# Kernel optimization log

Hardware: AMD Instinct MI355X
Metric: run time of the kernel (lower is better)

The kernel has to match this reference:

```python
import jax, jax.numpy as jnp
import numpy as np

B, S = 16384, 2048
EPS = 1e-8


def _autocorr(x, lag):
    # Pearson correlation between x[:, :-lag] and x[:, lag:] (ddof cancels).
    a = x[:, :-lag]
    b = x[:, lag:]
    am = a.mean(axis=1, keepdims=True)
    bm = b.mean(axis=1, keepdims=True)
    cov = ((a - am) * (b - bm)).mean(axis=1)
    return cov / (a.std(axis=1) * b.std(axis=1))


def _stat_features(x):
    S_len = x.shape[1]
    mean = x.mean(axis=1)
    xc = x - mean[:, None]
    m2 = (xc ** 2).mean(axis=1)
    m3 = (xc ** 3).mean(axis=1)
    m4 = (xc ** 4).mean(axis=1)
    std = jnp.sqrt(m2)
    min_v = x.min(axis=1)
    max_v = x.max(axis=1)
    q = jnp.percentile(x, jnp.array([25.0, 50.0, 75.0]), axis=1)  # [3, B]
    p25, median, p75 = q[0], q[1], q[2]
    diff = jnp.diff(x, axis=1)
    std_diff = diff.std(axis=1)
    trend = std_diff / (std + EPS)
    ac1 = _autocorr(x, 1)
    ac7 = _autocorr(x, 7)
    ac24 = _autocorr(x, 24)
    cv = std / (jnp.abs(mean) + EPS)
    iqr = p75 - p25
    seasonal = x[:, ::24].var(axis=1) / (m2 + EPS)
    skew = m3 / (m2 ** 1.5)          # scipy.stats.skew, bias=True
    kurt = m4 / (m2 ** 2) - 3.0      # scipy.stats.kurtosis, Fisher, bias=True
    length = jnp.full_like(mean, float(S_len))
    sum_abs_diff = jnp.abs(diff).sum(axis=1)
    mean_abs_diff = jnp.abs(diff).mean(axis=1)
    feats = jnp.stack([mean, std, min_v, max_v, median, trend, ac1, ac7, ac24,
                       cv, iqr, seasonal, skew, kurt, length,
                       sum_abs_diff, mean_abs_diff, std_diff, p25, p75], axis=1)
    return jnp.where(jnp.isfinite(feats), feats, 0.0)


def setup_inputs() -> dict:
    key = jax.random.key(0)
    k0, k1, k2, k3, k4 = jax.random.split(key, 5)
    x = jax.random.normal(k0, (B, S), dtype=jnp.float32)
    W1 = jax.random.normal(k1, (64, 20), dtype=jnp.float32) * 0.1
    b1 = jnp.zeros((64,), dtype=jnp.float32)
    W2 = jax.random.normal(k3, (128, 64), dtype=jnp.float32) * 0.1
    b2 = jnp.zeros((128,), dtype=jnp.float32)
    return {"x": x, "W1": W1, "b1": b1, "W2": W2, "b2": b2}


def reference(x, W1, b1, W2, b2):
    feats = _stat_features(x)                      # [B, 20]
    h = jax.nn.relu(feats @ W1.T + b1)             # [B, 64] (dropout inactive at eval)
    return h @ W2.T + b2                           # [B, 128]
```

## Files before the change

### kernel.cpp

```cpp
#include <hip/hip_runtime.h>
#include <cmath>

constexpr int S_LEN = 2048;
constexpr float EPS = 1e-8f;

typedef unsigned uvec32 __attribute__((ext_vector_type(32)));

__device__ __forceinline__ float fin(float v) { return isfinite(v) ? v : 0.0f; }
__device__ __forceinline__ float rcpf(float x) { return __builtin_amdgcn_rcpf(x); }

__device__ __forceinline__ unsigned f2o_bits(unsigned u) {
    return (u & 0x80000000u) ? ~u : (u | 0x80000000u);
}
__device__ __forceinline__ float o2f(unsigned u) {
    return __uint_as_float((u & 0x80000000u) ? (u ^ 0x80000000u) : ~u);
}

template <int Ctrl, int Rmask>
__device__ __forceinline__ int dpp_zero_i(int x) {
    return __builtin_amdgcn_update_dpp(0, x, Ctrl, Rmask, 0xF, true);
}
template <int Ctrl>
__device__ __forceinline__ int dpp_keep_i(int x) {
    return __builtin_amdgcn_update_dpp(x, x, Ctrl, 0xF, 0xF, false);
}
__device__ __forceinline__ float dpp_shdn1_f(float x) {
    return __uint_as_float((unsigned)dpp_zero_i<0x130, 0xF>((int)__float_as_uint(x)));
}
__device__ __forceinline__ int wred_add_i(int v) {
    v += dpp_zero_i<0xB1, 0xF>(v);
    v += dpp_zero_i<0x4E, 0xF>(v);
    v += dpp_zero_i<0x114, 0xF>(v);
    v += dpp_zero_i<0x118, 0xF>(v);
    v += dpp_zero_i<0x142, 0xA>(v);
    v += dpp_zero_i<0x143, 0xC>(v);
    return __builtin_amdgcn_readlane(v, 63);
}
__device__ __forceinline__ float wred_add_f(float v) {
    #define ADDF(CT, RM) v += __uint_as_float((unsigned)dpp_zero_i<CT, RM>((int)__float_as_uint(v)))
    ADDF(0xB1, 0xF); ADDF(0x4E, 0xF); ADDF(0x114, 0xF);
    ADDF(0x118, 0xF); ADDF(0x142, 0xA); ADDF(0x143, 0xC);
    #undef ADDF
    return __uint_as_float((unsigned)__builtin_amdgcn_readlane((int)__float_as_uint(v), 63));
}
__device__ __forceinline__ float wred_min_f(float v) {
    #define MINF(CT) v = fminf(v, __uint_as_float((unsigned)dpp_keep_i<CT>((int)__float_as_uint(v))))
    MINF(0xB1); MINF(0x4E); MINF(0x114); MINF(0x118); MINF(0x142); MINF(0x143);
    #undef MINF
    return __uint_as_float((unsigned)__builtin_amdgcn_readlane((int)__float_as_uint(v), 63));
}
__device__ __forceinline__ float wred_max_f(float v) {
    #define MAXF(CT) v = fmaxf(v, __uint_as_float((unsigned)dpp_keep_i<CT>((int)__float_as_uint(v))))
    MAXF(0xB1); MAXF(0x4E); MAXF(0x114); MAXF(0x118); MAXF(0x142); MAXF(0x143);
    #undef MAXF
    return __uint_as_float((unsigned)__builtin_amdgcn_readlane((int)__float_as_uint(v), 63));
}
__device__ __forceinline__ unsigned wred_umin(unsigned v) {
    #define MINU(CT) { unsigned t = (unsigned)dpp_keep_i<CT>((int)v); v = v < t ? v : t; }
    MINU(0xB1) MINU(0x4E) MINU(0x114) MINU(0x118) MINU(0x142) MINU(0x143)
    #undef MINU
    return (unsigned)__builtin_amdgcn_readlane((int)v, 63);
}
__device__ __forceinline__ float readlane_f(float x, int l) {
    return __uint_as_float((unsigned)__builtin_amdgcn_readlane((int)__float_as_uint(x), l));
}

__device__ __forceinline__ void transpose32(uvec32& A) {
    #pragma unroll
    for (int k = 0; k < 16; k++) {
        unsigned lo = __builtin_amdgcn_perm(A[k], A[k + 16], 0x07060302u);
        unsigned hi = __builtin_amdgcn_perm(A[k], A[k + 16], 0x05040100u);
        A[k] = lo; A[k + 16] = hi;
    }
    #pragma unroll
    for (int k0 = 0; k0 < 32; k0 += 16) {
        #pragma unroll
        for (int k = k0; k < k0 + 8; k++) {
            unsigned lo = __builtin_amdgcn_perm(A[k], A[k + 8], 0x07030501u);
            unsigned hi = __builtin_amdgcn_perm(A[k], A[k + 8], 0x06020400u);
            A[k] = lo; A[k + 8] = hi;
        }
    }
    #pragma unroll
    for (int j = 4; j; j >>= 1) {
        const unsigned m = (j == 4) ? 0x0F0F0F0Fu : (j == 2) ? 0x33333333u : 0x55555555u;
        #pragma unroll
        for (int k = 0; k < 32; k++) {
            if (!(k & j)) {
                unsigned Ak = A[k], Bk = A[k | j];
                A[k]     = ((Bk >> j) & m) | (Ak & ~m);
                A[k | j] = ((Ak << j) & ~m) | (Bk & m);
            }
        }
    }
}

#define VF(e) __uint_as_float(a[e])

__global__ __launch_bounds__(256) void transpose_w_kernel(
    const float* __restrict__ W1, float* __restrict__ wt)
{
    int tid = blockIdx.x * blockDim.x + threadIdx.x;
    int stride = gridDim.x * blockDim.x;
    for (int n = tid; n < 64 * 20; n += stride) {
        int j = n & 63, k = n >> 6;
        wt[n] = W1[j * 20 + k];
    }
}

__global__ __launch_bounds__(256, 5) void fused_stats_mlp_kernel(
    const float* __restrict__ x, const float* __restrict__ wt,
    const float* __restrict__ b1, const float* __restrict__ W2,
    const float* __restrict__ b2, float* __restrict__ out, int nrows)
{
    __shared__ __align__(16) float sf[4][20];
    __shared__ __align__(16) float hsh[4][64];

    const int gw   = (blockIdx.x * 256 + threadIdx.x) >> 6;
    const int lane = threadIdx.x & 63;
    const int w    = (threadIdx.x >> 6);
    if (gw >= nrows) return;

    uvec32 a;
    const float* xr = x + (size_t)gw * S_LEN + lane * 32;
    #pragma unroll
    for (int q = 0; q < 8; q++) {
        float4 t = reinterpret_cast<const float4*>(xr)[q];
        a[4 * q + 0] = __float_as_uint(t.x); a[4 * q + 1] = __float_as_uint(t.y);
        a[4 * q + 2] = __float_as_uint(t.z); a[4 * q + 3] = __float_as_uint(t.w);
    }

    float s1 = 0.f, s2 = 0.f, s3 = 0.f, s4 = 0.f, sd2 = 0.f, sad = 0.f;
    float p1 = 0.f, p7 = 0.f, p24 = 0.f, se1 = 0.f, se2 = 0.f;
    float mn = VF(0), mx = VF(0);
    #pragma unroll
    for (int e = 0; e < 32; e++) {
        float val = VF(e);
        float t = val * val;
        s1 += val; s2 += t;
        s3 = fmaf(t, val, s3); s4 = fmaf(t, t, s4);
        mn = fminf(mn, val); mx = fmaxf(mx, val);
    }
    #pragma unroll
    for (int e = 0; e < 31; e++) {
        float d = VF(e + 1) - VF(e);
        sd2 = fmaf(d, d, sd2); sad += fabsf(d);
        p1 = fmaf(VF(e), VF(e + 1), p1);
    }
    #pragma unroll
    for (int e = 0; e < 25; e++) p7 = fmaf(VF(e), VF(e + 7), p7);
    #pragma unroll
    for (int e = 0; e < 8; e++)  p24 = fmaf(VF(e), VF(e + 24), p24);

    const bool notlast = (lane < 63);
    #pragma unroll
    for (int j = 0; j < 24; j++) {
        float g = dpp_shdn1_f(VF(j));
        p24 = fmaf(VF(8 + j), g, p24);
        if (j < 7) p7 = fmaf(VF(25 + j), g, p7);
        if (j == 0) {
            float d = g - VF(31);
            float dm = notlast ? d : 0.f;
            sd2 = fmaf(dm, dm, sd2); sad += fabsf(dm);
            p1 = fmaf(VF(31), g, p1);
        }
    }
    {
        int r3 = lane % 3;
        float sv = (r3 == 0) ? VF(0) : ((r3 == 1) ? VF(16) : VF(8));
        se1 += sv; se2 = fmaf(sv, sv, se2);
        if (r3 == 0) { se1 += VF(24); se2 = fmaf(VF(24), VF(24), se2); }
    }
    const bool is63 = (lane == 63);
    float acc1 = 0.f, acc2 = 0.f, ck1 = 0.f, ck2 = 0.f;
    #pragma unroll
    for (int i = 0; i < 24; i++) {
        float pick = is63 ? VF(31 - i) : VF(i);
        acc1 += pick; acc2 = fmaf(pick, pick, acc2);
        if (i == 6) { ck1 = acc1; ck2 = acc2; }
    }
    const float h1  = readlane_f(VF(0), 0),   t1  = readlane_f(VF(31), 63);
    const float h7  = readlane_f(ck1, 0),     hq7 = readlane_f(ck2, 0);
    const float h24 = readlane_f(acc1, 0),    hq24 = readlane_f(acc2, 0);
    const float t7  = readlane_f(ck1, 63),    tq7 = readlane_f(ck2, 63);
    const float t24 = readlane_f(acc1, 63),   tq24 = readlane_f(acc2, 63);
    const float hq1 = h1 * h1, tq1 = t1 * t1;

    float S1  = wred_add_f(s1);
    float S2  = wred_add_f(s2);
    float S3  = wred_add_f(s3);
    float S4  = wred_add_f(s4);
    float SD2 = wred_add_f(sd2);
    float SAD = wred_add_f(sad);
    float P1  = wred_add_f(p1);
    float P7  = wred_add_f(p7);
    float P24 = wred_add_f(p24);
    float SE1 = wred_add_f(se1);
    float SE2 = wred_add_f(se2);
    float MN  = wred_min_f(mn);
    float MX  = wred_max_f(mx);

    {
        constexpr float invS  = 1.0f / 2048.0f;
        constexpr float invND = 1.0f / 2047.0f;
        const float Sf = (float)S_LEN;
        float mu = S1 * invS;
        float q2 = S2 * invS, q3 = S3 * invS, q4 = S4 * invS;
        float mu2 = mu * mu;
        float m2v = q2 - mu2;
        float m3v = q3 - 3.f * mu * q2 + 2.f * mu * mu2;
        float m4v = q4 - 4.f * mu * q3 + 6.f * mu2 * q2 - 3.f * mu2 * mu2;
        float stdv = sqrtf(m2v);
        float dmean = (t1 - h1) * invND;
        float dvar = SD2 * invND - dmean * dmean;
        float std_diff = sqrtf(fmaxf(dvar, 0.f));
        float trend = std_diff * rcpf(stdv + EPS);
        float ac[3];
        const float invN[3] = {1.0f / 2047.0f, 1.0f / 2041.0f, 1.0f / 2024.0f};
        const float Ps[3] = {P1, P7, P24};
        const float hd[3] = {h1, h7, h24},   hqv[3] = {hq1, hq7, hq24};
        const float tl[3] = {t1, t7, t24},   tqv[3] = {tq1, tq7, tq24};
        #pragma unroll
        for (int q = 0; q < 3; q++) {
            float in = invN[q];
            float sa = S1 - tl[q], sb = S1 - hd[q];
            float qa = S2 - tqv[q], qb = S2 - hqv[q];
            float am = sa * in, bm = sb * in;
            float cov = Ps[q] * in - am * bm;
            float as_ = sqrtf(fmaxf(qa * in - am * am, 0.f));
            float bs_ = sqrtf(fmaxf(qb * in - bm * bm, 0.f));
            ac[q] = cov * rcpf(as_ * bs_);
        }
        float cv = stdv * rcpf(fabsf(mu) + EPS);
        float sm = SE1 * (1.0f / 86.0f);
        float svar = SE2 * (1.0f / 86.0f) - sm * sm;
        float seasonal = svar * rcpf(m2v + EPS);
        float skew = m3v * rcpf(m2v * stdv);
        float kurt = m4v * rcpf(m2v * m2v) - 3.f;
        if (lane == 0) {
            float* s = sf[w];
            s[0]  = fin(mu);       s[1]  = fin(stdv);
            s[2]  = fin(MN);       s[3]  = fin(MX);
            s[5]  = fin(trend);    s[6]  = fin(ac[0]);
            s[7]  = fin(ac[1]);    s[8]  = fin(ac[2]);
            s[9]  = fin(cv);       s[11] = fin(seasonal);
            s[12] = fin(skew);     s[13] = fin(kurt);
            s[14] = Sf;            s[15] = fin(SAD);
            s[16] = fin(SAD * invND); s[17] = fin(std_diff);
        }
    }

    #pragma unroll
    for (int e = 0; e < 32; e++) a[e] = f2o_bits(a[e]);
    transpose32(a);

    unsigned act0 = ~0u, act1 = ~0u, act2 = ~0u;
    int K0 = 511, K1 = 1023, K2 = 1535;
    int cnt0 = 2048, cnt1 = 2048, cnt2 = 2048;
    unsigned uK0 = 0, uK1 = 0, uK2 = 0;
    #pragma unroll
    for (int b = 31; b >= 0; b--) {
        unsigned mb = a[31 - b];
        unsigned w0 = act0 & mb, w1 = act1 & mb, w2 = act2 & mb;
        int O01 = wred_add_i(__popc(w0) | (__popc(w1) << 16));
        int O2  = wred_add_i(__popc(w2));
        int c0 = cnt0 - (O01 & 0xFFFF);
        int c1 = cnt1 - (int)((unsigned)O01 >> 16);
        int c2i = cnt2 - O2;
        bool t0 = (K0 >= c0), t1c = (K1 >= c1), t2c = (K2 >= c2i);
        act0 = t0  ? w0 : (act0 ^ w0);
        act1 = t1c ? w1 : (act1 ^ w1);
        act2 = t2c ? w2 : (act2 ^ w2);
        cnt0 = t0  ? (cnt0 - c0)  : c0;
        cnt1 = t1c ? (cnt1 - c1)  : c1;
        cnt2 = t2c ? (cnt2 - c2i) : c2i;
        K0 = t0  ? (K0 - c0)  : K0;
        K1 = t1c ? (K1 - c1)  : K1;
        K2 = t2c ? (K2 - c2i) : K2;
        uK0 |= t0  ? (1u << b) : 0u;
        uK1 |= t1c ? (1u << b) : 0u;
        uK2 |= t2c ? (1u << b) : 0u;
    }
    const int eq0 = cnt0, eq1 = cnt1, eq2 = cnt2;

    transpose32(a);
    const unsigned k0p1 = uK0 + 1, k1p1 = uK1 + 1, k2p1 = uK2 + 1;
    unsigned m0 = ~0u, m1 = ~0u, m2 = ~0u;
    #pragma unroll
    for (int e = 0; e < 32; e++) {
        unsigned ue = a[e];
        unsigned d0 = ue - k0p1; m0 = m0 < d0 ? m0 : d0;
        unsigned d1 = ue - k1p1; m1 = m1 < d1 ? m1 : d1;
        unsigned d2 = ue - k2p1; m2 = m2 < d2 ? m2 : d2;
    }
    m0 = wred_umin(m0) + k0p1;
    m1 = wred_umin(m1) + k1p1;
    m2 = wred_umin(m2) + k2p1;

    float v511 = o2f(uK0), v1023 = o2f(uK1), v1535 = o2f(uK2);
    float v512  = (K0 + 1 < eq0) ? v511  : o2f(m0);
    float v1024 = (K1 + 1 < eq1) ? v1023 : o2f(m1);
    float v1536 = (K2 + 1 < eq2) ? v1535 : o2f(m2);
    float p25 = v511 + 0.75f * (v512 - v511);
    float med = 0.5f * (v1023 + v1024);
    float p75 = v1535 + 0.25f * (v1536 - v1535);
    float iqr = p75 - p25;

    if (lane == 0) {
        float* s = sf[w];
        s[4]  = fin(med); s[10] = fin(iqr);
        s[18] = fin(p25); s[19] = fin(p75);
    }
    __asm__ volatile("s_waitcnt lgkmcnt(0)" ::: "memory");
    __builtin_amdgcn_sched_barrier(0);

    const float* W1T = wt;
    const float4* sfv = (const float4*)sf[w];
    float4 f0 = sfv[0], f1 = sfv[1], f2 = sfv[2], f3 = sfv[3], f4 = sfv[4];
    float h = b1[lane];
    h = fmaf(f0.x, W1T[ 0 * 64 + lane], h);
    h = fmaf(f0.y, W1T[ 1 * 64 + lane], h);
    h = fmaf(f0.z, W1T[ 2 * 64 + lane], h);
    h = fmaf(f0.w, W1T[ 3 * 64 + lane], h);
    h = fmaf(f1.x, W1T[ 4 * 64 + lane], h);
    h = fmaf(f1.y, W1T[ 5 * 64 + lane], h);
    h = fmaf(f1.z, W1T[ 6 * 64 + lane], h);
    h = fmaf(f1.w, W1T[ 7 * 64 + lane], h);
    h = fmaf(f2.x, W1T[ 8 * 64 + lane], h);
    h = fmaf(f2.y, W1T[ 9 * 64 + lane], h);
    h = fmaf(f2.z, W1T[10 * 64 + lane], h);
    h = fmaf(f2.w, W1T[11 * 64 + lane], h);
    h = fmaf(f3.x, W1T[12 * 64 + lane], h);
    h = fmaf(f3.y, W1T[13 * 64 + lane], h);
    h = fmaf(f3.z, W1T[14 * 64 + lane], h);
    h = fmaf(f3.w, W1T[15 * 64 + lane], h);
    h = fmaf(f4.x, W1T[16 * 64 + lane], h);
    h = fmaf(f4.y, W1T[17 * 64 + lane], h);
    h = fmaf(f4.z, W1T[18 * 64 + lane], h);
    h = fmaf(f4.w, W1T[19 * 64 + lane], h);
    h = fmaxf(h, 0.f);
    hsh[w][lane] = h;
    __asm__ volatile("s_waitcnt lgkmcnt(0)" ::: "memory");
    __builtin_amdgcn_sched_barrier(0);

    const int j2 = lane * 2;
    float2 b2v = *(const float2*)(b2 + j2);
    float acc0 = b2v.x, acc1b = b2v.y;
    const float4* w2r0 = (const float4*)(W2 + (size_t)j2 * 64);
    const float4* w2r1 = (const float4*)(W2 + (size_t)(j2 + 1) * 64);
    const float4* hv4 = (const float4*)hsh[w];
    #pragma unroll
    for (int q = 0; q < 16; q++) {
        float4 hq = hv4[q];
        float4 wa = w2r0[q];
        float4 wb = w2r1[q];
        acc0 = fmaf(hq.x, wa.x, acc0); acc1b = fmaf(hq.x, wb.x, acc1b);
        acc0 = fmaf(hq.y, wa.y, acc0); acc1b = fmaf(hq.y, wb.y, acc1b);
        acc0 = fmaf(hq.z, wa.z, acc0); acc1b = fmaf(hq.z, wb.z, acc1b);
        acc0 = fmaf(hq.w, wa.w, acc0); acc1b = fmaf(hq.w, wb.w, acc1b);
    }
    *(float2*)(out + (size_t)gw * 128 + j2) = make_float2(acc0, acc1b);
}

extern "C" void kernel_launch(void* const* d_in, const int* in_sizes, int n_in,
                              void* d_out, int out_size, void* d_ws, size_t ws_size,
                              hipStream_t stream) {
    const float* x  = (const float*)d_in[0];
    const float* W1 = (const float*)d_in[1];
    const float* b1 = (const float*)d_in[2];
    const float* W2 = (const float*)d_in[3];
    const float* b2 = (const float*)d_in[4];
    float* out = (float*)d_out;
    float* wt  = (float*)d_ws;
    int nrows = in_sizes[0] / S_LEN;
    int blocks = (nrows + 3) / 4;
    transpose_w_kernel<<<2, 256, 0, stream>>>(W1, wt);
    fused_stats_mlp_kernel<<<blocks, 256, 0, stream>>>(x, wt, b1, W2, b2, out, nrows);
}
```

Before: 266.4 us.

## Process two rows per wavefront with interleaved radix select and early exit

Each wavefront now loads and processes two rows, and the bitwise radix-select passes for both rows are interleaved so their cross-lane reductions can overlap and hide latency. The bit loop exits early once every quantile candidate set has shrunk to one element, and an extra min-distance pass snaps the partial prefix to the actual element value. Launch bounds drop to 4 waves per SIMD because holding two 32-element rows in registers raises register pressure, and half as many blocks are launched.

```diff
diff --git a/kernel.cpp b/kernel.cpp
--- a/kernel.cpp
+++ b/kernel.cpp
@@ -95,47 +95,15 @@
     }
 }
 
-#define VF(e) __uint_as_float(a[e])
-
-__global__ __launch_bounds__(256) void transpose_w_kernel(
-    const float* __restrict__ W1, float* __restrict__ wt)
-{
-    int tid = blockIdx.x * blockDim.x + threadIdx.x;
-    int stride = gridDim.x * blockDim.x;
-    for (int n = tid; n < 64 * 20; n += stride) {
-        int j = n & 63, k = n >> 6;
-        wt[n] = W1[j * 20 + k];
-    }
-}
-
-__global__ __launch_bounds__(256, 5) void fused_stats_mlp_kernel(
-    const float* __restrict__ x, const float* __restrict__ wt,
-    const float* __restrict__ b1, const float* __restrict__ W2,
-    const float* __restrict__ b2, float* __restrict__ out, int nrows)
-{
-    __shared__ __align__(16) float sf[4][20];
-    __shared__ __align__(16) float hsh[4][64];
-
-    const int gw   = (blockIdx.x * 256 + threadIdx.x) >> 6;
-    const int lane = threadIdx.x & 63;
-    const int w    = (threadIdx.x >> 6);
-    if (gw >= nrows) return;
-
-    uvec32 a;
-    const float* xr = x + (size_t)gw * S_LEN + lane * 32;
-    #pragma unroll
-    for (int q = 0; q < 8; q++) {
-        float4 t = reinterpret_cast<const float4*>(xr)[q];
-        a[4 * q + 0] = __float_as_uint(t.x); a[4 * q + 1] = __float_as_uint(t.y);
-        a[4 * q + 2] = __float_as_uint(t.z); a[4 * q + 3] = __float_as_uint(t.w);
-    }
-
+#define AF(e) __uint_as_float(a[e])
+
+__device__ __forceinline__ void phase1_stats(const uvec32& a, float* s, int lane) {
     float s1 = 0.f, s2 = 0.f, s3 = 0.f, s4 = 0.f, sd2 = 0.f, sad = 0.f;
     float p1 = 0.f, p7 = 0.f, p24 = 0.f, se1 = 0.f, se2 = 0.f;
-    float mn = VF(0), mx = VF(0);
+    float mn = AF(0), mx = AF(0);
     #pragma unroll
     for (int e = 0; e < 32; e++) {
-        float val = VF(e);
+        float val = AF(e);
         float t = val * val;
         s1 += val; s2 += t;
         s3 = fmaf(t, val, s3); s4 = fmaf(t, t, s4);
@@ -143,43 +111,43 @@
     }
     #pragma unroll
     for (int e = 0; e < 31; e++) {
-        float d = VF(e + 1) - VF(e);
+        float d = AF(e + 1) - AF(e);
         sd2 = fmaf(d, d, sd2); sad += fabsf(d);
-        p1 = fmaf(VF(e), VF(e + 1), p1);
-    }
-    #pragma unroll
-    for (int e = 0; e < 25; e++) p7 = fmaf(VF(e), VF(e + 7), p7);
-    #pragma unroll
-    for (int e = 0; e < 8; e++)  p24 = fmaf(VF(e), VF(e + 24), p24);
+        p1 = fmaf(AF(e), AF(e + 1), p1);
+    }
+    #pragma unroll
+    for (int e = 0; e < 25; e++) p7 = fmaf(AF(e), AF(e + 7), p7);
+    #pragma unroll
+    for (int e = 0; e < 8; e++)  p24 = fmaf(AF(e), AF(e + 24), p24);
 
     const bool notlast = (lane < 63);
     #pragma unroll
     for (int j = 0; j < 24; j++) {
-        float g = dpp_shdn1_f(VF(j));
-        p24 = fmaf(VF(8 + j), g, p24);
-        if (j < 7) p7 = fmaf(VF(25 + j), g, p7);
+        float g = dpp_shdn1_f(AF(j));
+        p24 = fmaf(AF(8 + j), g, p24);
+        if (j < 7) p7 = fmaf(AF(25 + j), g, p7);
         if (j == 0) {
-            float d = g - VF(31);
+            float d = g - AF(31);
             float dm = notlast ? d : 0.f;
             sd2 = fmaf(dm, dm, sd2); sad += fabsf(dm);
-            p1 = fmaf(VF(31), g, p1);
+            p1 = fmaf(AF(31), g, p1);
         }
     }
     {
         int r3 = lane % 3;
-        float sv = (r3 == 0) ? VF(0) : ((r3 == 1) ? VF(16) : VF(8));
+        float sv = (r3 == 0) ? AF(0) : ((r3 == 1) ? AF(16) : AF(8));
         se1 += sv; se2 = fmaf(sv, sv, se2);
-        if (r3 == 0) { se1 += VF(24); se2 = fmaf(VF(24), VF(24), se2); }
+        if (r3 == 0) { se1 += AF(24); se2 = fmaf(AF(24), AF(24), se2); }
     }
     const bool is63 = (lane == 63);
     float acc1 = 0.f, acc2 = 0.f, ck1 = 0.f, ck2 = 0.f;
     #pragma unroll
     for (int i = 0; i < 24; i++) {
-        float pick = is63 ? VF(31 - i) : VF(i);
+        float pick = is63 ? AF(31 - i) : AF(i);
         acc1 += pick; acc2 = fmaf(pick, pick, acc2);
         if (i == 6) { ck1 = acc1; ck2 = acc2; }
     }
-    const float h1  = readlane_f(VF(0), 0),   t1  = readlane_f(VF(31), 63);
+    const float h1  = readlane_f(AF(0), 0),   t1  = readlane_f(AF(31), 63);
     const float h7  = readlane_f(ck1, 0),     hq7 = readlane_f(ck2, 0);
     const float h24 = readlane_f(acc1, 0),    hq24 = readlane_f(acc2, 0);
     const float t7  = readlane_f(ck1, 63),    tq7 = readlane_f(ck2, 63);
@@ -200,146 +168,84 @@
     float MN  = wred_min_f(mn);
     float MX  = wred_max_f(mx);
 
-    {
-        constexpr float invS  = 1.0f / 2048.0f;
-        constexpr float invND = 1.0f / 2047.0f;
-        const float Sf = (float)S_LEN;
-        float mu = S1 * invS;
-        float q2 = S2 * invS, q3 = S3 * invS, q4 = S4 * invS;
-        float mu2 = mu * mu;
-        float m2v = q2 - mu2;
-        float m3v = q3 - 3.f * mu * q2 + 2.f * mu * mu2;
-        float m4v = q4 - 4.f * mu * q3 + 6.f * mu2 * q2 - 3.f * mu2 * mu2;
-        float stdv = sqrtf(m2v);
-        float dmean = (t1 - h1) * invND;
-        float dvar = SD2 * invND - dmean * dmean;
-        float std_diff = sqrtf(fmaxf(dvar, 0.f));
-        float trend = std_diff * rcpf(stdv + EPS);
-        float ac[3];
-        const float invN[3] = {1.0f / 2047.0f, 1.0f / 2041.0f, 1.0f / 2024.0f};
-        const float Ps[3] = {P1, P7, P24};
-        const float hd[3] = {h1, h7, h24},   hqv[3] = {hq1, hq7, hq24};
-        const float tl[3] = {t1, t7, t24},   tqv[3] = {tq1, tq7, tq24};
-        #pragma unroll
-        for (int q = 0; q < 3; q++) {
-            float in = invN[q];
-            float sa = S1 - tl[q], sb = S1 - hd[q];
-            float qa = S2 - tqv[q], qb = S2 - hqv[q];
-            float am = sa * in, bm = sb * in;
-            float cov = Ps[q] * in - am * bm;
-            float as_ = sqrtf(fmaxf(qa * in - am * am, 0.f));
-            float bs_ = sqrtf(fmaxf(qb * in - bm * bm, 0.f));
-            ac[q] = cov * rcpf(as_ * bs_);
-        }
-        float cv = stdv * rcpf(fabsf(mu) + EPS);
-        float sm = SE1 * (1.0f / 86.0f);
-        float svar = SE2 * (1.0f / 86.0f) - sm * sm;
-        float seasonal = svar * rcpf(m2v + EPS);
-        float skew = m3v * rcpf(m2v * stdv);
-        float kurt = m4v * rcpf(m2v * m2v) - 3.f;
-        if (lane == 0) {
-            float* s = sf[w];
-            s[0]  = fin(mu);       s[1]  = fin(stdv);
-            s[2]  = fin(MN);       s[3]  = fin(MX);
-            s[5]  = fin(trend);    s[6]  = fin(ac[0]);
-            s[7]  = fin(ac[1]);    s[8]  = fin(ac[2]);
-            s[9]  = fin(cv);       s[11] = fin(seasonal);
-            s[12] = fin(skew);     s[13] = fin(kurt);
-            s[14] = Sf;            s[15] = fin(SAD);
-            s[16] = fin(SAD * invND); s[17] = fin(std_diff);
-        }
-    }
-
-    #pragma unroll
-    for (int e = 0; e < 32; e++) a[e] = f2o_bits(a[e]);
-    transpose32(a);
-
-    unsigned act0 = ~0u, act1 = ~0u, act2 = ~0u;
-    int K0 = 511, K1 = 1023, K2 = 1535;
-    int cnt0 = 2048, cnt1 = 2048, cnt2 = 2048;
-    unsigned uK0 = 0, uK1 = 0, uK2 = 0;
-    #pragma unroll
-    for (int b = 31; b >= 0; b--) {
-        unsigned mb = a[31 - b];
-        unsigned w0 = act0 & mb, w1 = act1 & mb, w2 = act2 & mb;
-        int O01 = wred_add_i(__popc(w0) | (__popc(w1) << 16));
-        int O2  = wred_add_i(__popc(w2));
-        int c0 = cnt0 - (O01 & 0xFFFF);
-        int c1 = cnt1 - (int)((unsigned)O01 >> 16);
-        int c2i = cnt2 - O2;
-        bool t0 = (K0 >= c0), t1c = (K1 >= c1), t2c = (K2 >= c2i);
-        act0 = t0  ? w0 : (act0 ^ w0);
-        act1 = t1c ? w1 : (act1 ^ w1);
-        act2 = t2c ? w2 : (act2 ^ w2);
-        cnt0 = t0  ? (cnt0 - c0)  : c0;
-        cnt1 = t1c ? (cnt1 - c1)  : c1;
-        cnt2 = t2c ? (cnt2 - c2i) : c2i;
-        K0 = t0  ? (K0 - c0)  : K0;
-        K1 = t1c ? (K1 - c1)  : K1;
-        K2 = t2c ? (K2 - c2i) : K2;
-        uK0 |= t0  ? (1u << b) : 0u;
-        uK1 |= t1c ? (1u << b) : 0u;
-        uK2 |= t2c ? (1u << b) : 0u;
-    }
-    const int eq0 = cnt0, eq1 = cnt1, eq2 = cnt2;
-
-    transpose32(a);
-    const unsigned k0p1 = uK0 + 1, k1p1 = uK1 + 1, k2p1 = uK2 + 1;
-    unsigned m0 = ~0u, m1 = ~0u, m2 = ~0u;
-    #pragma unroll
-    for (int e = 0; e < 32; e++) {
-        unsigned ue = a[e];
-        unsigned d0 = ue - k0p1; m0 = m0 < d0 ? m0 : d0;
-        unsigned d1 = ue - k1p1; m1 = m1 < d1 ? m1 : d1;
-        unsigned d2 = ue - k2p1; m2 = m2 < d2 ? m2 : d2;
-    }
-    m0 = wred_umin(m0) + k0p1;
-    m1 = wred_umin(m1) + k1p1;
-    m2 = wred_umin(m2) + k2p1;
-
-    float v511 = o2f(uK0), v1023 = o2f(uK1), v1535 = o2f(uK2);
-    float v512  = (K0 + 1 < eq0) ? v511  : o2f(m0);
-    float v1024 = (K1 + 1 < eq1) ? v1023 : o2f(m1);
-    float v1536 = (K2 + 1 < eq2) ? v1535 : o2f(m2);
-    float p25 = v511 + 0.75f * (v512 - v511);
-    float med = 0.5f * (v1023 + v1024);
-    float p75 = v1535 + 0.25f * (v1536 - v1535);
-    float iqr = p75 - p25;
-
+    constexpr float invS  = 1.0f / 2048.0f;
+    constexpr float invND = 1.0f / 2047.0f;
+    const float Sf = (float)S_LEN;
+    float mu = S1 * invS;
+    float q2 = S2 * invS, q3 = S3 * invS, q4 = S4 * invS;
+    float mu2 = mu * mu;
+    float m2v = q2 - mu2;
+    float m3v = q3 - 3.f * mu * q2 + 2.f * mu * mu2;
+    float m4v = q4 - 4.f * mu * q3 + 6.f * mu2 * q2 - 3.f * mu2 * mu2;
+    float stdv = sqrtf(m2v);
+    float dmean = (t1 - h1) * invND;
+    float dvar = SD2 * invND - dmean * dmean;
+    float std_diff = sqrtf(fmaxf(dvar, 0.f));
+    float trend = std_diff * rcpf(stdv + EPS);
+    float ac[3];
+    const float invN[3] = {1.0f / 2047.0f, 1.0f / 2041.0f, 1.0f / 2024.0f};
+    const float Ps[3] = {P1, P7, P24};
+    const float hd[3] = {h1, h7, h24},   hqv[3] = {hq1, hq7, hq24};
+    const float tl[3] = {t1, t7, t24},   tqv[3] = {tq1, tq7, tq24};
+    #pragma unroll
+    for (int q = 0; q < 3; q++) {
+        float in = invN[q];
+        float sa = S1 - tl[q], sb = S1 - hd[q];
+        float qa = S2 - tqv[q], qb = S2 - hqv[q];
+        float am = sa * in, bm = sb * in;
+        float cov = Ps[q] * in - am * bm;
+        float as_ = sqrtf(fmaxf(qa * in - am * am, 0.f));
+        float bs_ = sqrtf(fmaxf(qb * in - bm * bm, 0.f));
+        ac[q] = cov * rcpf(as_ * bs_);
+    }
+    float cv = stdv * rcpf(fabsf(mu) + EPS);
+    float sm = SE1 * (1.0f / 86.0f);
+    float svar = SE2 * (1.0f / 86.0f) - sm * sm;
+    float seasonal = svar * rcpf(m2v + EPS);
+    float skew = m3v * rcpf(m2v * stdv);
+    float kurt = m4v * rcpf(m2v * m2v) - 3.f;
     if (lane == 0) {
-        float* s = sf[w];
-        s[4]  = fin(med); s[10] = fin(iqr);
-        s[18] = fin(p25); s[19] = fin(p75);
-    }
-    __asm__ volatile("s_waitcnt lgkmcnt(0)" ::: "memory");
-    __builtin_amdgcn_sched_barrier(0);
-
-    const float* W1T = wt;
-    const float4* sfv = (const float4*)sf[w];
+        s[0]  = fin(mu);       s[1]  = fin(stdv);
+        s[2]  = fin(MN);       s[3]  = fin(MX);
+        s[5]  = fin(trend);    s[6]  = fin(ac[0]);
+        s[7]  = fin(ac[1]);    s[8]  = fin(ac[2]);
+        s[9]  = fin(cv);       s[11] = fin(seasonal);
+        s[12] = fin(skew);     s[13] = fin(kurt);
+        s[14] = Sf;            s[15] = fin(SAD);
+        s[16] = fin(SAD * invND); s[17] = fin(std_diff);
+    }
+}
+
+__device__ __forceinline__ void mlp_row(
+    const float* __restrict__ wt, const float* __restrict__ b1,
+    const float* __restrict__ W2, const float* __restrict__ b2,
+    const float* sfrow, float* hrow, float* __restrict__ outrow, int lane)
+{
+    const float4* sfv = (const float4*)sfrow;
     float4 f0 = sfv[0], f1 = sfv[1], f2 = sfv[2], f3 = sfv[3], f4 = sfv[4];
     float h = b1[lane];
-    h = fmaf(f0.x, W1T[ 0 * 64 + lane], h);
-    h = fmaf(f0.y, W1T[ 1 * 64 + lane], h);
-    h = fmaf(f0.z, W1T[ 2 * 64 + lane], h);
-    h = fmaf(f0.w, W1T[ 3 * 64 + lane], h);
-    h = fmaf(f1.x, W1T[ 4 * 64 + lane], h);
-    h = fmaf(f1.y, W1T[ 5 * 64 + lane], h);
-    h = fmaf(f1.z, W1T[ 6 * 64 + lane], h);
-    h = fmaf(f1.w, W1T[ 7 * 64 + lane], h);
-    h = fmaf(f2.x, W1T[ 8 * 64 + lane], h);
-    h = fmaf(f2.y, W1T[ 9 * 64 + lane], h);
-    h = fmaf(f2.z, W1T[10 * 64 + lane], h);
-    h = fmaf(f2.w, W1T[11 * 64 + lane], h);
-    h = fmaf(f3.x, W1T[12 * 64 + lane], h);
-    h = fmaf(f3.y, W1T[13 * 64 + lane], h);
-    h = fmaf(f3.z, W1T[14 * 64 + lane], h);
-    h = fmaf(f3.w, W1T[15 * 64 + lane], h);
-    h = fmaf(f4.x, W1T[16 * 64 + lane], h);
-    h = fmaf(f4.y, W1T[17 * 64 + lane], h);
-    h = fmaf(f4.z, W1T[18 * 64 + lane], h);
-    h = fmaf(f4.w, W1T[19 * 64 + lane], h);
+    h = fmaf(f0.x, wt[ 0 * 64 + lane], h);
+    h = fmaf(f0.y, wt[ 1 * 64 + lane], h);
+    h = fmaf(f0.z, wt[ 2 * 64 + lane], h);
+    h = fmaf(f0.w, wt[ 3 * 64 + lane], h);
+    h = fmaf(f1.x, wt[ 4 * 64 + lane], h);
+    h = fmaf(f1.y, wt[ 5 * 64 + lane], h);
+    h = fmaf(f1.z, wt[ 6 * 64 + lane], h);
+    h = fmaf(f1.w, wt[ 7 * 64 + lane], h);
+    h = fmaf(f2.x, wt[ 8 * 64 + lane], h);
+    h = fmaf(f2.y, wt[ 9 * 64 + lane], h);
+    h = fmaf(f2.z, wt[10 * 64 + lane], h);
+    h = fmaf(f2.w, wt[11 * 64 + lane], h);
+    h = fmaf(f3.x, wt[12 * 64 + lane], h);
+    h = fmaf(f3.y, wt[13 * 64 + lane], h);
+    h = fmaf(f3.z, wt[14 * 64 + lane], h);
+    h = fmaf(f3.w, wt[15 * 64 + lane], h);
+    h = fmaf(f4.x, wt[16 * 64 + lane], h);
+    h = fmaf(f4.y, wt[17 * 64 + lane], h);
+    h = fmaf(f4.z, wt[18 * 64 + lane], h);
+    h = fmaf(f4.w, wt[19 * 64 + lane], h);
     h = fmaxf(h, 0.f);
-    hsh[w][lane] = h;
+    hrow[lane] = h;
     __asm__ volatile("s_waitcnt lgkmcnt(0)" ::: "memory");
     __builtin_amdgcn_sched_barrier(0);
 
@@ -348,7 +254,7 @@
     float acc0 = b2v.x, acc1b = b2v.y;
     const float4* w2r0 = (const float4*)(W2 + (size_t)j2 * 64);
     const float4* w2r1 = (const float4*)(W2 + (size_t)(j2 + 1) * 64);
-    const float4* hv4 = (const float4*)hsh[w];
+    const float4* hv4 = (const float4*)hrow;
     #pragma unroll
     for (int q = 0; q < 16; q++) {
         float4 hq = hv4[q];
@@ -359,7 +265,193 @@
         acc0 = fmaf(hq.z, wa.z, acc0); acc1b = fmaf(hq.z, wb.z, acc1b);
         acc0 = fmaf(hq.w, wa.w, acc0); acc1b = fmaf(hq.w, wb.w, acc1b);
     }
-    *(float2*)(out + (size_t)gw * 128 + j2) = make_float2(acc0, acc1b);
+    *(float2*)(outrow + j2) = make_float2(acc0, acc1b);
+}
+
+__global__ __launch_bounds__(256) void transpose_w_kernel(
+    const float* __restrict__ W1, float* __restrict__ wt)
+{
+    int tid = blockIdx.x * blockDim.x + threadIdx.x;
+    int stride = gridDim.x * blockDim.x;
+    for (int n = tid; n < 64 * 20; n += stride) {
+        int j = n & 63, k = n >> 6;
+        wt[n] = W1[j * 20 + k];
+    }
+}
+
+__global__ __launch_bounds__(256, 4) void fused_stats_mlp_kernel(
+    const float* __restrict__ x, const float* __restrict__ wt,
+    const float* __restrict__ b1, const float* __restrict__ W2,
+    const float* __restrict__ b2, float* __restrict__ out, int nrows)
+{
+    __shared__ __align__(16) float sf[4][2][20];
+    __shared__ __align__(16) float hsh[4][2][64];
+
+    const int lane = threadIdx.x & 63;
+    const int w    = threadIdx.x >> 6;
+    int base = (blockIdx.x * 4 + w) * 2;
+    int r0 = min(base, nrows - 1);
+    int r1 = min(base + 1, nrows - 1);
+
+    uvec32 a, c;
+    const float* xr0 = x + (size_t)r0 * S_LEN + lane * 32;
+    const float* xr1 = x + (size_t)r1 * S_LEN + lane * 32;
+    #pragma unroll
+    for (int q = 0; q < 8; q++) {
+        float4 t = reinterpret_cast<const float4*>(xr0)[q];
+        a[4 * q + 0] = __float_as_uint(t.x); a[4 * q + 1] = __float_as_uint(t.y);
+        a[4 * q + 2] = __float_as_uint(t.z); a[4 * q + 3] = __float_as_uint(t.w);
+    }
+    #pragma unroll
+    for (int q = 0; q < 8; q++) {
+        float4 t = reinterpret_cast<const float4*>(xr1)[q];
+        c[4 * q + 0] = __float_as_uint(t.x); c[4 * q + 1] = __float_as_uint(t.y);
+        c[4 * q + 2] = __float_as_uint(t.z); c[4 * q + 3] = __float_as_uint(t.w);
+    }
+
+    phase1_stats(a, sf[w][0], lane);
+    phase1_stats(c, sf[w][1], lane);
+
+    #pragma unroll
+    for (int e = 0; e < 32; e++) { a[e] = f2o_bits(a[e]); c[e] = f2o_bits(c[e]); }
+    transpose32(a);
+    transpose32(c);
+
+    unsigned actA0 = ~0u, actA1 = ~0u, actA2 = ~0u;
+    unsigned actB0 = ~0u, actB1 = ~0u, actB2 = ~0u;
+    int KA0 = 511, KA1 = 1023, KA2 = 1535;
+    int KB0 = 511, KB1 = 1023, KB2 = 1535;
+    int cA0 = 2048, cA1 = 2048, cA2 = 2048;
+    int cB0 = 2048, cB1 = 2048, cB2 = 2048;
+    unsigned uA0 = 0, uA1 = 0, uA2 = 0;
+    unsigned uB0 = 0, uB1 = 0, uB2 = 0;
+    bool alldone = false;
+    #pragma unroll
+    for (int b = 31; b >= 0; b--) {
+        if (!alldone) {
+            unsigned mbA = a[31 - b];
+            unsigned mbB = c[31 - b];
+            unsigned wA0 = actA0 & mbA, wA1 = actA1 & mbA, wA2 = actA2 & mbA;
+            unsigned wB0 = actB0 & mbB, wB1 = actB1 & mbB, wB2 = actB2 & mbB;
+            int OA01 = wred_add_i(__popc(wA0) | (__popc(wA1) << 16));
+            int OB01 = wred_add_i(__popc(wB0) | (__popc(wB1) << 16));
+            int OA2  = wred_add_i(__popc(wA2));
+            int OB2  = wred_add_i(__popc(wB2));
+            int zA0 = cA0 - (OA01 & 0xFFFF);
+            int zA1 = cA1 - (int)((unsigned)OA01 >> 16);
+            int zA2 = cA2 - OA2;
+            int zB0 = cB0 - (OB01 & 0xFFFF);
+            int zB1 = cB1 - (int)((unsigned)OB01 >> 16);
+            int zB2 = cB2 - OB2;
+            bool tA0 = (KA0 >= zA0), tA1 = (KA1 >= zA1), tA2 = (KA2 >= zA2);
+            bool tB0 = (KB0 >= zB0), tB1 = (KB1 >= zB1), tB2 = (KB2 >= zB2);
+            actA0 = tA0 ? wA0 : (actA0 ^ wA0);
+            actA1 = tA1 ? wA1 : (actA1 ^ wA1);
+            actA2 = tA2 ? wA2 : (actA2 ^ wA2);
+            actB0 = tB0 ? wB0 : (actB0 ^ wB0);
+            actB1 = tB1 ? wB1 : (actB1 ^ wB1);
+            actB2 = tB2 ? wB2 : (actB2 ^ wB2);
+            cA0 = tA0 ? (cA0 - zA0) : zA0;
+            cA1 = tA1 ? (cA1 - zA1) : zA1;
+            cA2 = tA2 ? (cA2 - zA2) : zA2;
+            cB0 = tB0 ? (cB0 - zB0) : zB0;
+            cB1 = tB1 ? (cB1 - zB1) : zB1;
+            cB2 = tB2 ? (cB2 - zB2) : zB2;
+            KA0 = tA0 ? (KA0 - zA0) : KA0;
+            KA1 = tA1 ? (KA1 - zA1) : KA1;
+            KA2 = tA2 ? (KA2 - zA2) : KA2;
+            KB0 = tB0 ? (KB0 - zB0) : KB0;
+            KB1 = tB1 ? (KB1 - zB1) : KB1;
+            KB2 = tB2 ? (KB2 - zB2) : KB2;
+            uA0 |= tA0 ? (1u << b) : 0u;
+            uA1 |= tA1 ? (1u << b) : 0u;
+            uA2 |= tA2 ? (1u << b) : 0u;
+            uB0 |= tB0 ? (1u << b) : 0u;
+            uB1 |= tB1 ? (1u << b) : 0u;
+            uB2 |= tB2 ? (1u << b) : 0u;
+            alldone = (cA0 == 1) && (cA1 == 1) && (cA2 == 1) &&
+                      (cB0 == 1) && (cB1 == 1) && (cB2 == 1);
+        }
+    }
+    const int eA0 = cA0, eA1 = cA1, eA2 = cA2;
+    const int eB0 = cB0, eB1 = cB1, eB2 = cB2;
+
+    transpose32(a);
+    transpose32(c);
+
+    {
+        unsigned dA0 = ~0u, dA1 = ~0u, dA2 = ~0u;
+        unsigned dB0 = ~0u, dB1 = ~0u, dB2 = ~0u;
+        #pragma unroll
+        for (int e = 0; e < 32; e++) {
+            unsigned ua = a[e], uc = c[e];
+            unsigned t0 = ua - uA0; dA0 = dA0 < t0 ? dA0 : t0;
+            unsigned t1 = ua - uA1; dA1 = dA1 < t1 ? dA1 : t1;
+            unsigned t2 = ua - uA2; dA2 = dA2 < t2 ? dA2 : t2;
+            unsigned t3 = uc - uB0; dB0 = dB0 < t3 ? dB0 : t3;
+            unsigned t4 = uc - uB1; dB1 = dB1 < t4 ? dB1 : t4;
+            unsigned t5 = uc - uB2; dB2 = dB2 < t5 ? dB2 : t5;
+        }
+        uA0 += wred_umin(dA0);
+        uB0 += wred_umin(dB0);
+        uA1 += wred_umin(dA1);
+        uB1 += wred_umin(dB1);
+        uA2 += wred_umin(dA2);
+        uB2 += wred_umin(dB2);
+    }
+
+    const unsigned kA0 = uA0 + 1, kA1 = uA1 + 1, kA2 = uA2 + 1;
+    const unsigned kB0 = uB0 + 1, kB1 = uB1 + 1, kB2 = uB2 + 1;
+    unsigned mA0 = ~0u, mA1 = ~0u, mA2 = ~0u;
+    unsigned mB0 = ~0u, mB1 = ~0u, mB2 = ~0u;
+    #pragma unroll
+    for (int e = 0; e < 32; e++) {
+        unsigned ua = a[e], uc = c[e];
+        unsigned t0 = ua - kA0; mA0 = mA0 < t0 ? mA0 : t0;
+        unsigned t1 = ua - kA1; mA1 = mA1 < t1 ? mA1 : t1;
+        unsigned t2 = ua - kA2; mA2 = mA2 < t2 ? mA2 : t2;
+        unsigned t3 = uc - kB0; mB0 = mB0 < t3 ? mB0 : t3;
+        unsigned t4 = uc - kB1; mB1 = mB1 < t4 ? mB1 : t4;
+        unsigned t5 = uc - kB2; mB2 = mB2 < t5 ? mB2 : t5;
+    }
+    mA0 = wred_umin(mA0) + kA0;
+    mB0 = wred_umin(mB0) + kB0;
+    mA1 = wred_umin(mA1) + kA1;
+    mB1 = wred_umin(mB1) + kB1;
+    mA2 = wred_umin(mA2) + kA2;
+    mB2 = wred_umin(mB2) + kB2;
+
+    if (lane == 0) {
+        {
+            float v511 = o2f(uA0), v1023 = o2f(uA1), v1535 = o2f(uA2);
+            float v512  = (KA0 + 1 < eA0) ? v511  : o2f(mA0);
+            float v1024 = (KA1 + 1 < eA1) ? v1023 : o2f(mA1);
+            float v1536 = (KA2 + 1 < eA2) ? v1535 : o2f(mA2);
+            float p25 = v511 + 0.75f * (v512 - v511);
+            float med = 0.5f * (v1023 + v1024);
+            float p75 = v1535 + 0.25f * (v1536 - v1535);
+            float* s = sf[w][0];
+            s[4]  = fin(med); s[10] = fin(p75 - p25);
+            s[18] = fin(p25); s[19] = fin(p75);
+        }
+        {
+            float v511 = o2f(uB0), v1023 = o2f(uB1), v1535 = o2f(uB2);
+            float v512  = (KB0 + 1 < eB0) ? v511  : o2f(mB0);
+            float v1024 = (KB1 + 1 < eB1) ? v1023 : o2f(mB1);
+            float v1536 = (KB2 + 1 < eB2) ? v1535 : o2f(mB2);
+            float p25 = v511 + 0.75f * (v512 - v511);
+            float med = 0.5f * (v1023 + v1024);
+            float p75 = v1535 + 0.25f * (v1536 - v1535);
+            float* s = sf[w][1];
+            s[4]  = fin(med); s[10] = fin(p75 - p25);
+            s[18] = fin(p25); s[19] = fin(p75);
+        }
+    }
+    __asm__ volatile("s_waitcnt lgkmcnt(0)" ::: "memory");
+    __builtin_amdgcn_sched_barrier(0);
+
+    mlp_row(wt, b1, W2, b2, sf[w][0], hsh[w][0], out + (size_t)r0 * 128, lane);
+    mlp_row(wt, b1, W2, b2, sf[w][1], hsh[w][1], out + (size_t)r1 * 128, lane);
 }
 
 extern "C" void kernel_launch(void* const* d_in, const int* in_sizes, int n_in,
@@ -373,7 +465,7 @@
     float* out = (float*)d_out;
     float* wt  = (float*)d_ws;
     int nrows = in_sizes[0] / S_LEN;
-    int blocks = (nrows + 3) / 4;
+    int blocks = (nrows + 7) / 8;
     transpose_w_kernel<<<2, 256, 0, stream>>>(W1, wt);
     fused_stats_mlp_kernel<<<blocks, 256, 0, stream>>>(x, wt, b1, W2, b2, out, nrows);
 }
```

New measurement: 298.5 us. +12.1%, slower.
